# Kernel tuning notes

Hardware: AMD Instinct MI355X
Metric: run time of the kernel (lower is better)

## Reference

```python
import jax, jax.numpy as jnp
import numpy as np

HEADS = 4
EPS = 1e-5

def _layernorm(x, g, b):
    mu = jnp.mean(x, axis=-1, keepdims=True)
    var = jnp.var(x, axis=-1, keepdims=True)
    return (x - mu) / jnp.sqrt(var + EPS) * g + b

def setup_inputs() -> dict:
    key = jax.random.key(0)
    ks = jax.random.split(key, 16)
    N, dim, k, G = 400000, 256, 1, 4096
    h = jax.random.normal(ks[0], (N, dim), dtype=jnp.float32)
    batch = jnp.sort(jax.random.randint(ks[1], (N,), 0, G).astype(jnp.int64))
    s = 1.0 / np.sqrt(dim)
    return {
        "h": h,
        "batch": batch,
        "num_graphs": G,
        "seed": jax.random.normal(ks[2], (k, dim), dtype=jnp.float32),
        "in_proj_w": jax.random.uniform(ks[3], (3 * dim, dim), minval=-s, maxval=s, dtype=jnp.float32),
        "in_proj_b": jnp.zeros((3 * dim,), jnp.float32),
        "out_w": jax.random.uniform(ks[4], (dim, dim), minval=-s, maxval=s, dtype=jnp.float32),
        "out_b": jnp.zeros((dim,), jnp.float32),
        "w1": jax.random.uniform(ks[5], (4 * dim, dim), minval=-s, maxval=s, dtype=jnp.float32),
        "b1": jnp.zeros((4 * dim,), jnp.float32),
        "w2": jax.random.uniform(ks[6], (dim, 4 * dim), minval=-1.0 / np.sqrt(4 * dim), maxval=1.0 / np.sqrt(4 * dim), dtype=jnp.float32),
        "b2": jnp.zeros((dim,), jnp.float32),
        "g1": jnp.ones((dim,), jnp.float32),
        "beta1": jnp.zeros((dim,), jnp.float32),
        "g2": jnp.ones((dim,), jnp.float32),
        "beta2": jnp.zeros((dim,), jnp.float32),
    }

def reference(h, batch, num_graphs, seed, in_proj_w, in_proj_b, out_w, out_b,
              w1, b1, w2, b2, g1, beta1, g2, beta2):
    N, dim = h.shape
    k = seed.shape[0]
    hd = dim // HEADS
    G = num_graphs
    # q/k/v projections (torch MHA packed in_proj: rows [0:dim]=Q, [dim:2dim]=K, [2dim:]=V)
    q = seed @ in_proj_w[:dim].T + in_proj_b[:dim]                 # [k, dim]
    kk = h @ in_proj_w[dim:2 * dim].T + in_proj_b[dim:2 * dim]     # [N, dim]
    vv = h @ in_proj_w[2 * dim:].T + in_proj_b[2 * dim:]           # [N, dim]
    qh = q.reshape(k, HEADS, hd).transpose(1, 0, 2)                # [H, k, hd]
    kh = kk.reshape(N, HEADS, hd)                                  # [N, H, hd]
    vh = vv.reshape(N, HEADS, hd)                                  # [N, H, hd]
    scale = 1.0 / np.sqrt(hd)
    scores = jnp.einsum('hkd,nhd->nhk', qh, kh) * scale            # [N, H, k]
    # segment softmax over nodes of each graph
    smax = jax.ops.segment_max(scores, batch, num_segments=G)      # [G, H, k]
    e = jnp.exp(scores - smax[batch])                              # [N, H, k]
    denom = jax.ops.segment_sum(e, batch, num_segments=G)          # [G, H, k]
    wv = jax.ops.segment_sum(e[:, :, :, None] * vh[:, :, None, :], batch, num_segments=G)  # [G, H, k, hd]
    attn = jnp.where(denom[..., None] > 0, wv / jnp.maximum(denom, 1e-9)[..., None], 0.0)
    attn = attn.transpose(0, 2, 1, 3).reshape(G, k, dim)           # [G, k, dim]
    o = attn @ out_w.T + out_b                                     # [G, k, dim]
    x = _layernorm(o + seed[None, :, :], g1, beta1)
    f = jax.nn.relu(x @ w1.T + b1) @ w2.T + b2
    x = _layernorm(x + f, g2, beta2)
    # empty graphs output zeros (matches torch loop)
    count = jax.ops.segment_sum(jnp.ones((N,), jnp.float32), batch, num_segments=G)
    return jnp.where((count > 0)[:, None, None], x, 0.0)
```

## Files before the change

### kernel.cpp

```cpp
#include <hip/hip_runtime.h>
#include <hip/hip_bf16.h>


#define DIM 256
#define CHUNK 32

#define OFF_C      0
#define OFF_D      1024
#define OFF_CONST  1028
#define OFF_P2     2048
#define OFF_T      264192
#define OFF_O      4458496
#define OFF_X1     5507072
#define OFF_CNT    6555648

__global__ __launch_bounds__(256) void prep1_kernel(
    const float* __restrict__ seed, const float* __restrict__ ipw,
    const float* __restrict__ ipb, const float* __restrict__ out_w,
    const float* __restrict__ out_b, float* __restrict__ cvec,
    float* __restrict__ dconst, float* __restrict__ constvec)
{
    const float scale = 0.125f;
    int t = threadIdx.x;
    __shared__ float q_s[DIM];
    float acc = ipb[t];
    for (int d = 0; d < DIM; ++d) acc += seed[d] * ipw[t * DIM + d];
    q_s[t] = acc;
    __syncthreads();
    for (int h = 0; h < 4; ++h) {
        float a = 0.f;
        for (int j = 0; j < 64; ++j)
            a += q_s[h * 64 + j] * ipw[(size_t)(DIM + h * 64 + j) * DIM + t];
        cvec[h * DIM + t] = a * scale;
    }
    if (t < 4) {
        float a = 0.f;
        for (int j = 0; j < 64; ++j)
            a += q_s[t * 64 + j] * ipb[DIM + t * 64 + j];
        dconst[t] = a * scale;
    }
    float cc = out_b[t];
    for (int c = 0; c < DIM; ++c)
        cc += out_w[t * DIM + c] * ipb[2 * DIM + c];
    constvec[t] = cc;
}

__global__ __launch_bounds__(256) void prep2_kernel(
    const float* __restrict__ ipw, const float* __restrict__ out_w,
    float* __restrict__ P2)
{
    int i = blockIdx.x;
    int h = blockIdx.y;
    int t = threadIdx.x;
    float a = 0.f;
    for (int j = 0; j < 64; ++j) {
        float w = out_w[i * DIM + h * 64 + j];
        a += w * ipw[(size_t)(2 * DIM + h * 64 + j) * DIM + t];
    }
    P2[(size_t)i * 1024 + h * DIM + t] = a;
}

__global__ __launch_bounds__(256) void attn_pool_kernel(
    const float* __restrict__ hmat, const int* __restrict__ batch,
    const float* __restrict__ cvec, const float* __restrict__ dconst,
    float* __restrict__ T, int* __restrict__ cnt, int N)
{
    int g = blockIdx.x;
    int tid = threadIdx.x;
    int lane = tid & 63, wave = tid >> 6;

    __shared__ float hbuf[CHUNK][DIM];
    __shared__ float4 esc[CHUNK];

    int s, e;
    { int l = 0, r = N;
      while (l < r) { int m = (l + r) >> 1; if (batch[m] < g) l = m + 1; else r = m; }
      s = l; }
    { int l = s, r = N;
      while (l < r) { int m = (l + r) >> 1; if (batch[m] < g + 1) l = m + 1; else r = m; }
      e = l; }

    if (tid == 0) cnt[g] = e - s;
    size_t tbase = (size_t)g * 1024;
    if (e == s) {
        T[tbase + tid] = 0.f; T[tbase + 256 + tid] = 0.f;
        T[tbase + 512 + tid] = 0.f; T[tbase + 768 + tid] = 0.f;
        return;
    }

    int hh = lane & 3, seg = lane >> 2;
    const float* cb = cvec + hh * DIM + seg * 16;
    float4 cr0 = *(const float4*)(cb + 0);
    float4 cr1 = *(const float4*)(cb + 4);
    float4 cr2 = *(const float4*)(cb + 8);
    float4 cr3 = *(const float4*)(cb + 12);
    float dc_mine = dconst[hh];

    float m0 = -1e30f, m1 = -1e30f, m2 = -1e30f, m3 = -1e30f;
    float l0 = 0.f, l1 = 0.f, l2 = 0.f, l3 = 0.f;
    float S0 = 0.f, S1 = 0.f, S2 = 0.f, S3 = 0.f;

    for (int n0 = s; n0 < e; n0 += CHUNK) {
        int ccnt = min(CHUNK, e - n0);
        for (int idx = tid; idx < ccnt * 64; idx += 256) {
            int j = idx >> 6, q4 = idx & 63;
            float4 v = *(const float4*)&hmat[(size_t)(n0 + j) * DIM + q4 * 4];
            *(float4*)&hbuf[j][q4 * 4] = v;
        }
        __syncthreads();

        for (int j = wave; j < ccnt; j += 4) {
            const float* hb = &hbuf[j][seg * 16];
            float4 h0 = *(const float4*)(hb + 0);
            float4 h1 = *(const float4*)(hb + 4);
            float4 h2 = *(const float4*)(hb + 8);
            float4 h3 = *(const float4*)(hb + 12);
            float p = h0.x * cr0.x + h0.y * cr0.y + h0.z * cr0.z + h0.w * cr0.w
                    + h1.x * cr1.x + h1.y * cr1.y + h1.z * cr1.z + h1.w * cr1.w
                    + h2.x * cr2.x + h2.y * cr2.y + h2.z * cr2.z + h2.w * cr2.w
                    + h3.x * cr3.x + h3.y * cr3.y + h3.z * cr3.z + h3.w * cr3.w;
            p += __shfl_xor(p, 4);
            p += __shfl_xor(p, 8);
            p += __shfl_xor(p, 16);
            p += __shfl_xor(p, 32);
            if (lane < 4) ((float*)&esc[j])[lane] = p + dc_mine;
        }
        __syncthreads();

        float cm0 = -1e30f, cm1 = -1e30f, cm2 = -1e30f, cm3 = -1e30f;
        for (int j = 0; j < ccnt; ++j) {
            float4 sc = esc[j];
            cm0 = fmaxf(cm0, sc.x); cm1 = fmaxf(cm1, sc.y);
            cm2 = fmaxf(cm2, sc.z); cm3 = fmaxf(cm3, sc.w);
        }
        float nm0 = fmaxf(m0, cm0), nm1 = fmaxf(m1, cm1);
        float nm2 = fmaxf(m2, cm2), nm3 = fmaxf(m3, cm3);
        float a0 = __expf(m0 - nm0), a1 = __expf(m1 - nm1);
        float a2 = __expf(m2 - nm2), a3 = __expf(m3 - nm3);
        __syncthreads();
        if (tid < ccnt * 4) {
            int hsel = tid & 3;
            float nm = (hsel == 0) ? nm0 : (hsel == 1) ? nm1 : (hsel == 2) ? nm2 : nm3;
            float* ep = (float*)esc;
            ep[tid] = __expf(ep[tid] - nm);
        }
        __syncthreads();

        S0 *= a0; S1 *= a1; S2 *= a2; S3 *= a3;
        l0 *= a0; l1 *= a1; l2 *= a2; l3 *= a3;
        for (int j = 0; j < ccnt; ++j) {
            float4 e4 = esc[j];
            float hv = hbuf[j][tid];
            S0 = fmaf(e4.x, hv, S0); S1 = fmaf(e4.y, hv, S1);
            S2 = fmaf(e4.z, hv, S2); S3 = fmaf(e4.w, hv, S3);
            l0 += e4.x; l1 += e4.y; l2 += e4.z; l3 += e4.w;
        }
        m0 = nm0; m1 = nm1; m2 = nm2; m3 = nm3;
        __syncthreads();
    }

    float i0 = (l0 > 0.f) ? 1.f / l0 : 0.f;
    float i1 = (l1 > 0.f) ? 1.f / l1 : 0.f;
    float i2 = (l2 > 0.f) ? 1.f / l2 : 0.f;
    float i3 = (l3 > 0.f) ? 1.f / l3 : 0.f;
    T[tbase + tid]       = S0 * i0;
    T[tbase + 256 + tid] = S1 * i1;
    T[tbase + 512 + tid] = S2 * i2;
    T[tbase + 768 + tid] = S3 * i3;
}

__global__ __launch_bounds__(256) void gemm_tn_kernel(
    const float* __restrict__ A, const float* __restrict__ B,
    const float* __restrict__ bias, float* __restrict__ C,
    int M, int N, int K, int relu)
{
    __shared__ float As[16][68];
    __shared__ float Bs[16][68];
    int tid = threadIdx.x;
    int m0 = blockIdx.x * 64, n0 = blockIdx.y * 64;
    int tm = (tid & 15) * 4, tn = (tid >> 4) * 4;
    int lr = tid >> 2;
    int lk = (tid & 3) * 4;
    const float* Ap = A + (size_t)(m0 + lr) * K + lk;
    const float* Bp = B + (size_t)(n0 + lr) * K + lk;
    float acc00=0,acc01=0,acc02=0,acc03=0, acc10=0,acc11=0,acc12=0,acc13=0;
    float acc20=0,acc21=0,acc22=0,acc23=0, acc30=0,acc31=0,acc32=0,acc33=0;

    for (int k0 = 0; k0 < K; k0 += 16) {
        float4 a4 = *(const float4*)(Ap + k0);
        float4 b4 = *(const float4*)(Bp + k0);
        __syncthreads();
        As[lk + 0][lr] = a4.x; As[lk + 1][lr] = a4.y;
        As[lk + 2][lr] = a4.z; As[lk + 3][lr] = a4.w;
        Bs[lk + 0][lr] = b4.x; Bs[lk + 1][lr] = b4.y;
        Bs[lk + 2][lr] = b4.z; Bs[lk + 3][lr] = b4.w;
        __syncthreads();
#pragma unroll
        for (int kk = 0; kk < 16; ++kk) {
            float4 av = *(const float4*)&As[kk][tm];
            float4 bv = *(const float4*)&Bs[kk][tn];
            acc00 = fmaf(av.x, bv.x, acc00); acc01 = fmaf(av.x, bv.y, acc01);
            acc02 = fmaf(av.x, bv.z, acc02); acc03 = fmaf(av.x, bv.w, acc03);
            acc10 = fmaf(av.y, bv.x, acc10); acc11 = fmaf(av.y, bv.y, acc11);
            acc12 = fmaf(av.y, bv.z, acc12); acc13 = fmaf(av.y, bv.w, acc13);
            acc20 = fmaf(av.z, bv.x, acc20); acc21 = fmaf(av.z, bv.y, acc21);
            acc22 = fmaf(av.z, bv.z, acc22); acc23 = fmaf(av.z, bv.w, acc23);
            acc30 = fmaf(av.w, bv.x, acc30); acc31 = fmaf(av.w, bv.y, acc31);
            acc32 = fmaf(av.w, bv.z, acc32); acc33 = fmaf(av.w, bv.w, acc33);
        }
    }
    float bb0 = bias[n0 + tn + 0], bb1 = bias[n0 + tn + 1];
    float bb2 = bias[n0 + tn + 2], bb3 = bias[n0 + tn + 3];
    float r00=acc00+bb0, r01=acc01+bb1, r02=acc02+bb2, r03=acc03+bb3;
    float r10=acc10+bb0, r11=acc11+bb1, r12=acc12+bb2, r13=acc13+bb3;
    float r20=acc20+bb0, r21=acc21+bb1, r22=acc22+bb2, r23=acc23+bb3;
    float r30=acc30+bb0, r31=acc31+bb1, r32=acc32+bb2, r33=acc33+bb3;
    if (relu) {
        r00=fmaxf(r00,0.f); r01=fmaxf(r01,0.f); r02=fmaxf(r02,0.f); r03=fmaxf(r03,0.f);
        r10=fmaxf(r10,0.f); r11=fmaxf(r11,0.f); r12=fmaxf(r12,0.f); r13=fmaxf(r13,0.f);
        r20=fmaxf(r20,0.f); r21=fmaxf(r21,0.f); r22=fmaxf(r22,0.f); r23=fmaxf(r23,0.f);
        r30=fmaxf(r30,0.f); r31=fmaxf(r31,0.f); r32=fmaxf(r32,0.f); r33=fmaxf(r33,0.f);
    }
    float4* Cp;
    Cp = (float4*)&C[(size_t)(m0 + tm + 0) * N + n0 + tn]; *Cp = make_float4(r00,r01,r02,r03);
    Cp = (float4*)&C[(size_t)(m0 + tm + 1) * N + n0 + tn]; *Cp = make_float4(r10,r11,r12,r13);
    Cp = (float4*)&C[(size_t)(m0 + tm + 2) * N + n0 + tn]; *Cp = make_float4(r20,r21,r22,r23);
    Cp = (float4*)&C[(size_t)(m0 + tm + 3) * N + n0 + tn]; *Cp = make_float4(r30,r31,r32,r33);
}

__global__ __launch_bounds__(256) void ln_kernel(
    const float* __restrict__ A, const float* __restrict__ Bv, int b_vec,
    const float* __restrict__ gam, const float* __restrict__ bet,
    const int* __restrict__ cnt, float* __restrict__ out)
{
    int g = blockIdx.x, t = threadIdx.x;
    int lane = t & 63, wave = t >> 6;
    float v = A[(size_t)g * DIM + t] + (b_vec ? Bv[t] : Bv[(size_t)g * DIM + t]);
    float s = v, q = v * v;
    for (int off = 32; off; off >>= 1) {
        s += __shfl_down(s, off);
        q += __shfl_down(q, off);
    }
    __shared__ float ss[4], qq[4];
    if (lane == 0) { ss[wave] = s; qq[wave] = q; }
    __syncthreads();
    s = ss[0] + ss[1] + ss[2] + ss[3];
    q = qq[0] + qq[1] + qq[2] + qq[3];
    float mu = s * (1.f / DIM);
    float var = q * (1.f / DIM) - mu * mu;
    float r = rsqrtf(fmaxf(var, 0.f) + 1e-5f);
    float y = (v - mu) * r * gam[t] + bet[t];
    if (cnt) y = (cnt[g] > 0) ? y : 0.f;
    out[(size_t)g * DIM + t] = y;
}

extern "C" void kernel_launch(void* const* d_in, const int* in_sizes, int n_in,
                              void* d_out, int out_size, void* d_ws, size_t ws_size,
                              hipStream_t stream) {
    const float* h     = (const float*)d_in[0];
    const int*   batch = (const int*)d_in[1];
    const float* seed  = (const float*)d_in[3];
    const float* ipw   = (const float*)d_in[4];
    const float* ipb   = (const float*)d_in[5];
    const float* out_w = (const float*)d_in[6];
    const float* out_b = (const float*)d_in[7];
    const float* w1    = (const float*)d_in[8];
    const float* b1    = (const float*)d_in[9];
    const float* w2    = (const float*)d_in[10];
    const float* b2    = (const float*)d_in[11];
    const float* g1    = (const float*)d_in[12];
    const float* be1   = (const float*)d_in[13];
    const float* g2    = (const float*)d_in[14];
    const float* be2   = (const float*)d_in[15];

    int N = in_sizes[1];
    int G = out_size / DIM;

    float* ws = (float*)d_ws;
    float* cvec     = ws + OFF_C;
    float* dconst   = ws + OFF_D;
    float* constvec = ws + OFF_CONST;
    float* P2       = ws + OFF_P2;
    float* T        = ws + OFF_T;
    float* obuf     = ws + OFF_O;
    float* x1       = ws + OFF_X1;
    int*   cnt      = (int*)(ws + OFF_CNT);

    prep1_kernel<<<1, 256, 0, stream>>>(seed, ipw, ipb, out_w, out_b,
                                        cvec, dconst, constvec);
    prep2_kernel<<<dim3(256, 4), 256, 0, stream>>>(ipw, out_w, P2);
    attn_pool_kernel<<<G, 256, 0, stream>>>(h, batch, cvec, dconst, T, cnt, N);
    gemm_tn_kernel<<<dim3(G / 64, 256 / 64), 256, 0, stream>>>(
        T, P2, constvec, obuf, G, 256, 1024, 0);
    ln_kernel<<<G, 256, 0, stream>>>(obuf, seed, 1, g1, be1, nullptr, x1);
    gemm_tn_kernel<<<dim3(G / 64, 1024 / 64), 256, 0, stream>>>(
        x1, w1, b1, T, G, 1024, 256, 1);
    gemm_tn_kernel<<<dim3(G / 64, 256 / 64), 256, 0, stream>>>(
        T, w2, b2, obuf, G, 256, 1024, 0);
    ln_kernel<<<G, 256, 0, stream>>>(x1, obuf, 0, g2, be2, cnt, (float*)d_out);
}
```

Before: 805.1 us.

## Use bf16 MFMA GEMMs with fused LayerNorm and simplify segment softmax

Replaces the fp32 LDS-tiled GEMMs with bf16 MFMA 16x16x32 kernels and folds both LayerNorms (and the empty-graph mask) into the GEMM epilogues. Weights are pre-converted to bf16 in a single merged prep kernel that also builds the fused projection matrices. The attention pooling drops the online max-rescaling and extra barriers, exponentiating scores directly and reducing denominators once at the end. This cuts launches, memory traffic and sync overhead, at the cost of bf16 precision and no overflow protection in the softmax.

```diff
diff --git a/kernel.cpp b/kernel.cpp
--- a/kernel.cpp
+++ b/kernel.cpp
@@ -5,65 +5,77 @@
 #define DIM 256
 #define CHUNK 32
 
+typedef short bf16x8 __attribute__((ext_vector_type(8)));
+typedef float f32x4  __attribute__((ext_vector_type(4)));
+#define MFMA16(a, b, c) __builtin_amdgcn_mfma_f32_16x16x32_bf16(a, b, c, 0, 0, 0)
+
 #define OFF_C      0
 #define OFF_D      1024
-#define OFF_CONST  1028
-#define OFF_P2     2048
-#define OFF_T      264192
-#define OFF_O      4458496
-#define OFF_X1     5507072
-#define OFF_CNT    6555648
-
-__global__ __launch_bounds__(256) void prep1_kernel(
+#define OFF_CONST  1040
+#define OFF_P2B    2048
+#define OFF_W1B    133120
+#define OFF_W2B    264192
+#define OFF_TB     395264
+#define OFF_X1     2492416
+#define OFF_X1B    3540992
+#define OFF_UB     4065280
+#define OFF_CNT    6162432
+
+__global__ __launch_bounds__(256) void prep_all_kernel(
     const float* __restrict__ seed, const float* __restrict__ ipw,
     const float* __restrict__ ipb, const float* __restrict__ out_w,
-    const float* __restrict__ out_b, float* __restrict__ cvec,
-    float* __restrict__ dconst, float* __restrict__ constvec)
-{
-    const float scale = 0.125f;
-    int t = threadIdx.x;
+    const float* __restrict__ out_b, const float* __restrict__ w1,
+    const float* __restrict__ w2,
+    float* __restrict__ cvec, float* __restrict__ dconst,
+    float* __restrict__ constvec, __hip_bfloat16* __restrict__ P2b,
+    __hip_bfloat16* __restrict__ w1b, __hip_bfloat16* __restrict__ w2b)
+{
+    int b = blockIdx.x, t = threadIdx.x;
     __shared__ float q_s[DIM];
-    float acc = ipb[t];
-    for (int d = 0; d < DIM; ++d) acc += seed[d] * ipw[t * DIM + d];
-    q_s[t] = acc;
-    __syncthreads();
-    for (int h = 0; h < 4; ++h) {
+    if (b < 1024) {
+        int i = b >> 2, hD = b & 3;
         float a = 0.f;
         for (int j = 0; j < 64; ++j)
-            a += q_s[h * 64 + j] * ipw[(size_t)(DIM + h * 64 + j) * DIM + t];
-        cvec[h * DIM + t] = a * scale;
-    }
-    if (t < 4) {
-        float a = 0.f;
-        for (int j = 0; j < 64; ++j)
-            a += q_s[t * 64 + j] * ipb[DIM + t * 64 + j];
-        dconst[t] = a * scale;
-    }
-    float cc = out_b[t];
-    for (int c = 0; c < DIM; ++c)
-        cc += out_w[t * DIM + c] * ipb[2 * DIM + c];
-    constvec[t] = cc;
-}
-
-__global__ __launch_bounds__(256) void prep2_kernel(
-    const float* __restrict__ ipw, const float* __restrict__ out_w,
-    float* __restrict__ P2)
-{
-    int i = blockIdx.x;
-    int h = blockIdx.y;
-    int t = threadIdx.x;
-    float a = 0.f;
-    for (int j = 0; j < 64; ++j) {
-        float w = out_w[i * DIM + h * 64 + j];
-        a += w * ipw[(size_t)(2 * DIM + h * 64 + j) * DIM + t];
-    }
-    P2[(size_t)i * 1024 + h * DIM + t] = a;
+            a += out_w[i * DIM + hD * 64 + j]
+               * ipw[(size_t)(2 * DIM + hD * 64 + j) * DIM + t];
+        P2b[(size_t)i * 1024 + hD * DIM + t] = __float2bfloat16(a);
+    } else if (b == 1024) {
+        const float scale = 0.125f;
+        float acc = ipb[t];
+        for (int d = 0; d < DIM; ++d) acc += seed[d] * ipw[t * DIM + d];
+        q_s[t] = acc;
+        __syncthreads();
+        for (int hh = 0; hh < 4; ++hh) {
+            float a = 0.f;
+            for (int j = 0; j < 64; ++j)
+                a += q_s[hh * 64 + j] * ipw[(size_t)(DIM + hh * 64 + j) * DIM + t];
+            cvec[hh * DIM + t] = a * scale;
+        }
+        if (t < 4) {
+            float a = 0.f;
+            for (int j = 0; j < 64; ++j)
+                a += q_s[t * 64 + j] * ipb[DIM + t * 64 + j];
+            dconst[t] = a * scale;
+        }
+        float cc = out_b[t];
+        for (int c = 0; c < DIM; ++c)
+            cc += out_w[t * DIM + c] * ipb[2 * DIM + c];
+        constvec[t] = cc;
+    } else if (b < 1153) {
+        int base = (b - 1025) * 2048 + t;
+        for (int i = 0; i < 8; ++i)
+            w1b[base + i * 256] = __float2bfloat16(w1[base + i * 256]);
+    } else {
+        int base = (b - 1153) * 2048 + t;
+        for (int i = 0; i < 8; ++i)
+            w2b[base + i * 256] = __float2bfloat16(w2[base + i * 256]);
+    }
 }
 
 __global__ __launch_bounds__(256) void attn_pool_kernel(
     const float* __restrict__ hmat, const int* __restrict__ batch,
     const float* __restrict__ cvec, const float* __restrict__ dconst,
-    float* __restrict__ T, int* __restrict__ cnt, int N)
+    __hip_bfloat16* __restrict__ Tb, int* __restrict__ cnt, int N)
 {
     int g = blockIdx.x;
     int tid = threadIdx.x;
@@ -71,6 +83,7 @@
 
     __shared__ float hbuf[CHUNK][DIM];
     __shared__ float4 esc[CHUNK];
+    __shared__ float lred[4][4];
 
     int s, e;
     { int l = 0, r = N;
@@ -83,8 +96,9 @@
     if (tid == 0) cnt[g] = e - s;
     size_t tbase = (size_t)g * 1024;
     if (e == s) {
-        T[tbase + tid] = 0.f; T[tbase + 256 + tid] = 0.f;
-        T[tbase + 512 + tid] = 0.f; T[tbase + 768 + tid] = 0.f;
+        __hip_bfloat16 z = __float2bfloat16(0.f);
+        Tb[tbase + tid] = z; Tb[tbase + 256 + tid] = z;
+        Tb[tbase + 512 + tid] = z; Tb[tbase + 768 + tid] = z;
         return;
     }
 
@@ -96,9 +110,8 @@
     float4 cr3 = *(const float4*)(cb + 12);
     float dc_mine = dconst[hh];
 
-    float m0 = -1e30f, m1 = -1e30f, m2 = -1e30f, m3 = -1e30f;
-    float l0 = 0.f, l1 = 0.f, l2 = 0.f, l3 = 0.f;
     float S0 = 0.f, S1 = 0.f, S2 = 0.f, S3 = 0.f;
+    float lp = 0.f;
 
     for (int n0 = s; n0 < e; n0 += CHUNK) {
         int ccnt = min(CHUNK, e - n0);
@@ -123,135 +136,186 @@
             p += __shfl_xor(p, 8);
             p += __shfl_xor(p, 16);
             p += __shfl_xor(p, 32);
-            if (lane < 4) ((float*)&esc[j])[lane] = p + dc_mine;
+            if (lane < 4) {
+                float ev = __expf(p + dc_mine);
+                ((float*)&esc[j])[lane] = ev;
+                lp += ev;
+            }
         }
         __syncthreads();
 
-        float cm0 = -1e30f, cm1 = -1e30f, cm2 = -1e30f, cm3 = -1e30f;
-        for (int j = 0; j < ccnt; ++j) {
-            float4 sc = esc[j];
-            cm0 = fmaxf(cm0, sc.x); cm1 = fmaxf(cm1, sc.y);
-            cm2 = fmaxf(cm2, sc.z); cm3 = fmaxf(cm3, sc.w);
-        }
-        float nm0 = fmaxf(m0, cm0), nm1 = fmaxf(m1, cm1);
-        float nm2 = fmaxf(m2, cm2), nm3 = fmaxf(m3, cm3);
-        float a0 = __expf(m0 - nm0), a1 = __expf(m1 - nm1);
-        float a2 = __expf(m2 - nm2), a3 = __expf(m3 - nm3);
-        __syncthreads();
-        if (tid < ccnt * 4) {
-            int hsel = tid & 3;
-            float nm = (hsel == 0) ? nm0 : (hsel == 1) ? nm1 : (hsel == 2) ? nm2 : nm3;
-            float* ep = (float*)esc;
-            ep[tid] = __expf(ep[tid] - nm);
-        }
-        __syncthreads();
-
-        S0 *= a0; S1 *= a1; S2 *= a2; S3 *= a3;
-        l0 *= a0; l1 *= a1; l2 *= a2; l3 *= a3;
         for (int j = 0; j < ccnt; ++j) {
             float4 e4 = esc[j];
             float hv = hbuf[j][tid];
             S0 = fmaf(e4.x, hv, S0); S1 = fmaf(e4.y, hv, S1);
             S2 = fmaf(e4.z, hv, S2); S3 = fmaf(e4.w, hv, S3);
-            l0 += e4.x; l1 += e4.y; l2 += e4.z; l3 += e4.w;
-        }
-        m0 = nm0; m1 = nm1; m2 = nm2; m3 = nm3;
+        }
         __syncthreads();
     }
 
-    float i0 = (l0 > 0.f) ? 1.f / l0 : 0.f;
-    float i1 = (l1 > 0.f) ? 1.f / l1 : 0.f;
-    float i2 = (l2 > 0.f) ? 1.f / l2 : 0.f;
-    float i3 = (l3 > 0.f) ? 1.f / l3 : 0.f;
-    T[tbase + tid]       = S0 * i0;
-    T[tbase + 256 + tid] = S1 * i1;
-    T[tbase + 512 + tid] = S2 * i2;
-    T[tbase + 768 + tid] = S3 * i3;
-}
-
-__global__ __launch_bounds__(256) void gemm_tn_kernel(
-    const float* __restrict__ A, const float* __restrict__ B,
-    const float* __restrict__ bias, float* __restrict__ C,
-    int M, int N, int K, int relu)
-{
-    __shared__ float As[16][68];
-    __shared__ float Bs[16][68];
-    int tid = threadIdx.x;
-    int m0 = blockIdx.x * 64, n0 = blockIdx.y * 64;
-    int tm = (tid & 15) * 4, tn = (tid >> 4) * 4;
-    int lr = tid >> 2;
-    int lk = (tid & 3) * 4;
-    const float* Ap = A + (size_t)(m0 + lr) * K + lk;
-    const float* Bp = B + (size_t)(n0 + lr) * K + lk;
-    float acc00=0,acc01=0,acc02=0,acc03=0, acc10=0,acc11=0,acc12=0,acc13=0;
-    float acc20=0,acc21=0,acc22=0,acc23=0, acc30=0,acc31=0,acc32=0,acc33=0;
-
-    for (int k0 = 0; k0 < K; k0 += 16) {
-        float4 a4 = *(const float4*)(Ap + k0);
-        float4 b4 = *(const float4*)(Bp + k0);
-        __syncthreads();
-        As[lk + 0][lr] = a4.x; As[lk + 1][lr] = a4.y;
-        As[lk + 2][lr] = a4.z; As[lk + 3][lr] = a4.w;
-        Bs[lk + 0][lr] = b4.x; Bs[lk + 1][lr] = b4.y;
-        Bs[lk + 2][lr] = b4.z; Bs[lk + 3][lr] = b4.w;
-        __syncthreads();
-#pragma unroll
-        for (int kk = 0; kk < 16; ++kk) {
-            float4 av = *(const float4*)&As[kk][tm];
-            float4 bv = *(const float4*)&Bs[kk][tn];
-            acc00 = fmaf(av.x, bv.x, acc00); acc01 = fmaf(av.x, bv.y, acc01);
-            acc02 = fmaf(av.x, bv.z, acc02); acc03 = fmaf(av.x, bv.w, acc03);
-            acc10 = fmaf(av.y, bv.x, acc10); acc11 = fmaf(av.y, bv.y, acc11);
-            acc12 = fmaf(av.y, bv.z, acc12); acc13 = fmaf(av.y, bv.w, acc13);
-            acc20 = fmaf(av.z, bv.x, acc20); acc21 = fmaf(av.z, bv.y, acc21);
-            acc22 = fmaf(av.z, bv.z, acc22); acc23 = fmaf(av.z, bv.w, acc23);
-            acc30 = fmaf(av.w, bv.x, acc30); acc31 = fmaf(av.w, bv.y, acc31);
-            acc32 = fmaf(av.w, bv.z, acc32); acc33 = fmaf(av.w, bv.w, acc33);
-        }
-    }
-    float bb0 = bias[n0 + tn + 0], bb1 = bias[n0 + tn + 1];
-    float bb2 = bias[n0 + tn + 2], bb3 = bias[n0 + tn + 3];
-    float r00=acc00+bb0, r01=acc01+bb1, r02=acc02+bb2, r03=acc03+bb3;
-    float r10=acc10+bb0, r11=acc11+bb1, r12=acc12+bb2, r13=acc13+bb3;
-    float r20=acc20+bb0, r21=acc21+bb1, r22=acc22+bb2, r23=acc23+bb3;
-    float r30=acc30+bb0, r31=acc31+bb1, r32=acc32+bb2, r33=acc33+bb3;
-    if (relu) {
-        r00=fmaxf(r00,0.f); r01=fmaxf(r01,0.f); r02=fmaxf(r02,0.f); r03=fmaxf(r03,0.f);
-        r10=fmaxf(r10,0.f); r11=fmaxf(r11,0.f); r12=fmaxf(r12,0.f); r13=fmaxf(r13,0.f);
-        r20=fmaxf(r20,0.f); r21=fmaxf(r21,0.f); r22=fmaxf(r22,0.f); r23=fmaxf(r23,0.f);
-        r30=fmaxf(r30,0.f); r31=fmaxf(r31,0.f); r32=fmaxf(r32,0.f); r33=fmaxf(r33,0.f);
-    }
-    float4* Cp;
-    Cp = (float4*)&C[(size_t)(m0 + tm + 0) * N + n0 + tn]; *Cp = make_float4(r00,r01,r02,r03);
-    Cp = (float4*)&C[(size_t)(m0 + tm + 1) * N + n0 + tn]; *Cp = make_float4(r10,r11,r12,r13);
-    Cp = (float4*)&C[(size_t)(m0 + tm + 2) * N + n0 + tn]; *Cp = make_float4(r20,r21,r22,r23);
-    Cp = (float4*)&C[(size_t)(m0 + tm + 3) * N + n0 + tn]; *Cp = make_float4(r30,r31,r32,r33);
-}
-
-__global__ __launch_bounds__(256) void ln_kernel(
-    const float* __restrict__ A, const float* __restrict__ Bv, int b_vec,
-    const float* __restrict__ gam, const float* __restrict__ bet,
-    const int* __restrict__ cnt, float* __restrict__ out)
-{
-    int g = blockIdx.x, t = threadIdx.x;
-    int lane = t & 63, wave = t >> 6;
-    float v = A[(size_t)g * DIM + t] + (b_vec ? Bv[t] : Bv[(size_t)g * DIM + t]);
-    float s = v, q = v * v;
-    for (int off = 32; off; off >>= 1) {
-        s += __shfl_down(s, off);
-        q += __shfl_down(q, off);
-    }
-    __shared__ float ss[4], qq[4];
-    if (lane == 0) { ss[wave] = s; qq[wave] = q; }
+    if (lane < 4) lred[wave][lane] = lp;
     __syncthreads();
-    s = ss[0] + ss[1] + ss[2] + ss[3];
-    q = qq[0] + qq[1] + qq[2] + qq[3];
-    float mu = s * (1.f / DIM);
-    float var = q * (1.f / DIM) - mu * mu;
-    float r = rsqrtf(fmaxf(var, 0.f) + 1e-5f);
-    float y = (v - mu) * r * gam[t] + bet[t];
-    if (cnt) y = (cnt[g] > 0) ? y : 0.f;
-    out[(size_t)g * DIM + t] = y;
+    float l0 = lred[0][0] + lred[1][0] + lred[2][0] + lred[3][0];
+    float l1 = lred[0][1] + lred[1][1] + lred[2][1] + lred[3][1];
+    float l2 = lred[0][2] + lred[1][2] + lred[2][2] + lred[3][2];
+    float l3 = lred[0][3] + lred[1][3] + lred[2][3] + lred[3][3];
+    Tb[tbase + tid]       = __float2bfloat16(S0 / l0);
+    Tb[tbase + 256 + tid] = __float2bfloat16(S1 / l1);
+    Tb[tbase + 512 + tid] = __float2bfloat16(S2 / l2);
+    Tb[tbase + 768 + tid] = __float2bfloat16(S3 / l3);
+}
+
+__global__ __launch_bounds__(64) void gemm_o_ln1_kernel(
+    const __hip_bfloat16* __restrict__ Tb, const __hip_bfloat16* __restrict__ P2b,
+    const float* __restrict__ constvec, const float* __restrict__ seed,
+    const float* __restrict__ g1, const float* __restrict__ be1,
+    float* __restrict__ x1, __hip_bfloat16* __restrict__ x1b)
+{
+    int m0 = blockIdx.x * 16;
+    int lane = threadIdx.x, quad = lane >> 4, l16 = lane & 15;
+    f32x4 acc[16];
+#pragma unroll
+    for (int i = 0; i < 16; ++i) acc[i] = (f32x4){0.f, 0.f, 0.f, 0.f};
+    const __hip_bfloat16* Ap = Tb + (size_t)(m0 + l16) * 1024 + quad * 8;
+    const __hip_bfloat16* Bp = P2b + (size_t)l16 * 1024 + quad * 8;
+    for (int k0 = 0; k0 < 1024; k0 += 32) {
+        bf16x8 a = *(const bf16x8*)(Ap + k0);
+#pragma unroll
+        for (int nt = 0; nt < 16; ++nt) {
+            bf16x8 b = *(const bf16x8*)(Bp + (size_t)nt * 16 * 1024 + k0);
+            acc[nt] = MFMA16(a, b, acc[nt]);
+        }
+    }
+    float v[16][4];
+    float sum[4] = {0, 0, 0, 0}, sq[4] = {0, 0, 0, 0};
+#pragma unroll
+    for (int nt = 0; nt < 16; ++nt) {
+        int col = nt * 16 + l16;
+        float cv = constvec[col] + seed[col];
+#pragma unroll
+        for (int r = 0; r < 4; ++r) {
+            float x = acc[nt][r] + cv;
+            v[nt][r] = x; sum[r] += x; sq[r] += x * x;
+        }
+    }
+    float mu_r[4], rs_r[4];
+#pragma unroll
+    for (int r = 0; r < 4; ++r) {
+        float s_ = sum[r], q_ = sq[r];
+        s_ += __shfl_xor(s_, 1);  q_ += __shfl_xor(q_, 1);
+        s_ += __shfl_xor(s_, 2);  q_ += __shfl_xor(q_, 2);
+        s_ += __shfl_xor(s_, 4);  q_ += __shfl_xor(q_, 4);
+        s_ += __shfl_xor(s_, 8);  q_ += __shfl_xor(q_, 8);
+        float mu = s_ * (1.f / 256);
+        float var = q_ * (1.f / 256) - mu * mu;
+        mu_r[r] = mu;
+        rs_r[r] = rsqrtf(fmaxf(var, 0.f) + 1e-5f);
+    }
+#pragma unroll
+    for (int nt = 0; nt < 16; ++nt) {
+        int col = nt * 16 + l16;
+        float gg = g1[col], bb = be1[col];
+#pragma unroll
+        for (int r = 0; r < 4; ++r) {
+            int gr = m0 + quad * 4 + r;
+            float y = (v[nt][r] - mu_r[r]) * rs_r[r] * gg + bb;
+            x1[(size_t)gr * 256 + col] = y;
+            x1b[(size_t)gr * 256 + col] = __float2bfloat16(y);
+        }
+    }
+}
+
+__global__ __launch_bounds__(64) void gemm_u_kernel(
+    const __hip_bfloat16* __restrict__ x1b, const __hip_bfloat16* __restrict__ w1b,
+    const float* __restrict__ b1, __hip_bfloat16* __restrict__ ub)
+{
+    int m0 = blockIdx.x * 16, nb0 = blockIdx.y * 128;
+    int lane = threadIdx.x, quad = lane >> 4, l16 = lane & 15;
+    f32x4 acc[8];
+#pragma unroll
+    for (int i = 0; i < 8; ++i) acc[i] = (f32x4){0.f, 0.f, 0.f, 0.f};
+    const __hip_bfloat16* Ap = x1b + (size_t)(m0 + l16) * 256 + quad * 8;
+    const __hip_bfloat16* Bp = w1b + (size_t)(nb0 + l16) * 256 + quad * 8;
+#pragma unroll
+    for (int k0 = 0; k0 < 256; k0 += 32) {
+        bf16x8 a = *(const bf16x8*)(Ap + k0);
+#pragma unroll
+        for (int nt = 0; nt < 8; ++nt) {
+            bf16x8 b = *(const bf16x8*)(Bp + (size_t)nt * 16 * 256 + k0);
+            acc[nt] = MFMA16(a, b, acc[nt]);
+        }
+    }
+#pragma unroll
+    for (int nt = 0; nt < 8; ++nt) {
+        int col = nb0 + nt * 16 + l16;
+        float bb = b1[col];
+#pragma unroll
+        for (int r = 0; r < 4; ++r) {
+            int gr = m0 + quad * 4 + r;
+            float y = fmaxf(acc[nt][r] + bb, 0.f);
+            ub[(size_t)gr * 1024 + col] = __float2bfloat16(y);
+        }
+    }
+}
+
+__global__ __launch_bounds__(64) void gemm_f_ln2_kernel(
+    const __hip_bfloat16* __restrict__ ub, const __hip_bfloat16* __restrict__ w2b,
+    const float* __restrict__ b2, const float* __restrict__ x1,
+    const float* __restrict__ g2, const float* __restrict__ be2,
+    const int* __restrict__ cnt, float* __restrict__ outp)
+{
+    int m0 = blockIdx.x * 16;
+    int lane = threadIdx.x, quad = lane >> 4, l16 = lane & 15;
+    f32x4 acc[16];
+#pragma unroll
+    for (int i = 0; i < 16; ++i) acc[i] = (f32x4){0.f, 0.f, 0.f, 0.f};
+    const __hip_bfloat16* Ap = ub + (size_t)(m0 + l16) * 1024 + quad * 8;
+    const __hip_bfloat16* Bp = w2b + (size_t)l16 * 1024 + quad * 8;
+    for (int k0 = 0; k0 < 1024; k0 += 32) {
+        bf16x8 a = *(const bf16x8*)(Ap + k0);
+#pragma unroll
+        for (int nt = 0; nt < 16; ++nt) {
+            bf16x8 b = *(const bf16x8*)(Bp + (size_t)nt * 16 * 1024 + k0);
+            acc[nt] = MFMA16(a, b, acc[nt]);
+        }
+    }
+    float v[16][4];
+    float sum[4] = {0, 0, 0, 0}, sq[4] = {0, 0, 0, 0};
+#pragma unroll
+    for (int nt = 0; nt < 16; ++nt) {
+        int col = nt * 16 + l16;
+        float bb = b2[col];
+#pragma unroll
+        for (int r = 0; r < 4; ++r) {
+            int gr = m0 + quad * 4 + r;
+            float x = acc[nt][r] + bb + x1[(size_t)gr * 256 + col];
+            v[nt][r] = x; sum[r] += x; sq[r] += x * x;
+        }
+    }
+    float mu_r[4], rs_r[4];
+#pragma unroll
+    for (int r = 0; r < 4; ++r) {
+        float s_ = sum[r], q_ = sq[r];
+        s_ += __shfl_xor(s_, 1);  q_ += __shfl_xor(q_, 1);
+        s_ += __shfl_xor(s_, 2);  q_ += __shfl_xor(q_, 2);
+        s_ += __shfl_xor(s_, 4);  q_ += __shfl_xor(q_, 4);
+        s_ += __shfl_xor(s_, 8);  q_ += __shfl_xor(q_, 8);
+        float mu = s_ * (1.f / 256);
+        float var = q_ * (1.f / 256) - mu * mu;
+        mu_r[r] = mu;
+        rs_r[r] = rsqrtf(fmaxf(var, 0.f) + 1e-5f);
+    }
+#pragma unroll
+    for (int r = 0; r < 4; ++r) {
+        int gr = m0 + quad * 4 + r;
+        float mask = (cnt[gr] > 0) ? 1.f : 0.f;
+#pragma unroll
+        for (int nt = 0; nt < 16; ++nt) {
+            int col = nt * 16 + l16;
+            float y = ((v[nt][r] - mu_r[r]) * rs_r[r] * g2[col] + be2[col]) * mask;
+            outp[(size_t)gr * 256 + col] = y;
+        }
+    }
 }
 
 extern "C" void kernel_launch(void* const* d_in, const int* in_sizes, int n_in,
@@ -280,22 +344,21 @@
     float* cvec     = ws + OFF_C;
     float* dconst   = ws + OFF_D;
     float* constvec = ws + OFF_CONST;
-    float* P2       = ws + OFF_P2;
-    float* T        = ws + OFF_T;
-    float* obuf     = ws + OFF_O;
+    __hip_bfloat16* P2b = (__hip_bfloat16*)(ws + OFF_P2B);
+    __hip_bfloat16* w1b = (__hip_bfloat16*)(ws + OFF_W1B);
+    __hip_bfloat16* w2b = (__hip_bfloat16*)(ws + OFF_W2B);
+    __hip_bfloat16* Tb  = (__hip_bfloat16*)(ws + OFF_TB);
     float* x1       = ws + OFF_X1;
+    __hip_bfloat16* x1b = (__hip_bfloat16*)(ws + OFF_X1B);
+    __hip_bfloat16* ub  = (__hip_bfloat16*)(ws + OFF_UB);
     int*   cnt      = (int*)(ws + OFF_CNT);
 
-    prep1_kernel<<<1, 256, 0, stream>>>(seed, ipw, ipb, out_w, out_b,
-                                        cvec, dconst, constvec);
-    prep2_kernel<<<dim3(256, 4), 256, 0, stream>>>(ipw, out_w, P2);
-    attn_pool_kernel<<<G, 256, 0, stream>>>(h, batch, cvec, dconst, T, cnt, N);
-    gemm_tn_kernel<<<dim3(G / 64, 256 / 64), 256, 0, stream>>>(
-        T, P2, constvec, obuf, G, 256, 1024, 0);
-    ln_kernel<<<G, 256, 0, stream>>>(obuf, seed, 1, g1, be1, nullptr, x1);
-    gemm_tn_kernel<<<dim3(G / 64, 1024 / 64), 256, 0, stream>>>(
-        x1, w1, b1, T, G, 1024, 256, 1);
-    gemm_tn_kernel<<<dim3(G / 64, 256 / 64), 256, 0, stream>>>(
-        T, w2, b2, obuf, G, 256, 1024, 0);
-    ln_kernel<<<G, 256, 0, stream>>>(x1, obuf, 0, g2, be2, cnt, (float*)d_out);
-}
+    prep_all_kernel<<<1281, 256, 0, stream>>>(seed, ipw, ipb, out_w, out_b, w1, w2,
+                                              cvec, dconst, constvec, P2b, w1b, w2b);
+    attn_pool_kernel<<<G, 256, 0, stream>>>(h, batch, cvec, dconst, Tb, cnt, N);
+    gemm_o_ln1_kernel<<<G / 16, 64, 0, stream>>>(Tb, P2b, constvec, seed, g1, be1,
+                                                 x1, x1b);
+    gemm_u_kernel<<<dim3(G / 16, 8), 64, 0, stream>>>(x1b, w1b, b1, ub);
+    gemm_f_ln2_kernel<<<G / 16, 64, 0, stream>>>(ub, w2b, b2, x1, g2, be2, cnt,
+                                                 (float*)d_out);
+}
```

Result: faster. 716.2 us (-11.0%).
